# Performance work log

Hardware: AMD Instinct MI355X
Metric: run time of the kernel (lower is better)

Reference implementation:

```python
import jax, jax.numpy as jnp
import numpy as np

B, T, D = 2, 2048, 1024
NH, DH = 16, 64  # inner = NH*DH = D
SCALE_INIT = 0.02


def setup_inputs() -> dict:
    key = jax.random.key(0)
    kx, kq, kk, kv, ko = jax.random.split(key, 5)
    return {
        "x": jax.random.normal(kx, (B, T, D), dtype=jnp.float32),
        "Wq": jax.random.normal(kq, (D, NH * DH), dtype=jnp.float32) * SCALE_INIT,
        "Wk": jax.random.normal(kk, (D, NH * DH), dtype=jnp.float32) * SCALE_INIT,
        "Wv": jax.random.normal(kv, (D, NH * DH), dtype=jnp.float32) * SCALE_INIT,
        "Wo": jax.random.normal(ko, (NH * DH, D), dtype=jnp.float32) * SCALE_INIT,
    }


def reference(x, Wq, Wk, Wv, Wo):
    # x: (B, T, D)
    b, t, _ = x.shape

    def split_heads(h):
        # (B, T, NH*DH) -> (B, NH, T, DH)
        return h.reshape(b, t, NH, DH).transpose(0, 2, 1, 3)

    q = split_heads(x @ Wq)
    k = split_heads(x @ Wk)
    v = split_heads(x @ Wv)

    scale = jnp.asarray(1.0 / np.sqrt(DH), dtype=x.dtype)
    # The per-chunk loop in the original is mathematically equivalent to
    # full causal attention: each query row attends to keys with k_pos <= q_pos.
    scores = jnp.einsum("bhqd,bhkd->bhqk", q, k) * scale  # (B, NH, T, T)
    causal_mask = jnp.arange(t)[None, :] > jnp.arange(t)[:, None]  # k_pos > q_pos
    scores = jnp.where(causal_mask, -jnp.inf, scores)
    attn = jax.nn.softmax(scores, axis=-1)
    attn = jnp.nan_to_num(attn)  # matches torch.nan_to_num (no fully-masked rows in causal case)
    o = jnp.einsum("bhqk,bhkd->bhqd", attn, v)  # (B, NH, T, DH)
    o = o.transpose(0, 2, 1, 3).reshape(b, t, NH * DH)  # merge heads
    return o @ Wo  # (B, T, D)
```

## Files before the change

kernel.cpp:

```cpp
#include <hip/hip_runtime.h>
#include <hip/hip_bf16.h>
#include <string.h>

#define Bsz 2
#define Tsz 2048
#define Dsz 1024
#define NHsz 16
#define Msz (Bsz*Tsz)

typedef unsigned short bfu;
typedef __attribute__((ext_vector_type(8))) short short8;
typedef __attribute__((ext_vector_type(4))) short short4v;
typedef __attribute__((ext_vector_type(4))) float floatx4;

__device__ __forceinline__ bfu f2bf(float f) {
  unsigned int u = __builtin_bit_cast(unsigned int, f);
  u += 0x7fffu + ((u >> 16) & 1u);
  return (bfu)(u >> 16);
}

__device__ __forceinline__ short4v pack4bf(float a, float b, float c_, float d) {
  __hip_bfloat162 h01 = __float22bfloat162_rn(make_float2(a, b));
  __hip_bfloat162 h23 = __float22bfloat162_rn(make_float2(c_, d));
  uint2 uu;
  memcpy(&uu.x, &h01, 4);
  memcpy(&uu.y, &h23, 4);
  return __builtin_bit_cast(short4v, uu);
}

__device__ __forceinline__ short8 pack8bf(float4 a, float4 b) {
  __hip_bfloat162 h0 = __float22bfloat162_rn(make_float2(a.x, a.y));
  __hip_bfloat162 h1 = __float22bfloat162_rn(make_float2(a.z, a.w));
  __hip_bfloat162 h2 = __float22bfloat162_rn(make_float2(b.x, b.y));
  __hip_bfloat162 h3 = __float22bfloat162_rn(make_float2(b.z, b.w));
  uint4 u;
  memcpy(&u.x, &h0, 4); memcpy(&u.y, &h1, 4);
  memcpy(&u.z, &h2, 4); memcpy(&u.w, &h3, 4);
  return __builtin_bit_cast(short8, u);
}

__device__ __forceinline__ void async16(const void* g, void* l) {
  void* gnc = (void*)g;
  __builtin_amdgcn_global_load_lds((__attribute__((address_space(1))) void*)gnc,
                                   (__attribute__((address_space(3))) void*)l,
                                   16, 0, 0);
}

__global__ __launch_bounds__(256) void transpose_w(const float* __restrict__ W0, const float* __restrict__ W1,
                                                   const float* __restrict__ W2, const float* __restrict__ W3,
                                                   bfu* __restrict__ wt) {
  __shared__ float tile[32][33];
  const float* W = blockIdx.z == 0 ? W0 : blockIdx.z == 1 ? W1 : blockIdx.z == 2 ? W2 : W3;
  const float s = (blockIdx.z == 0) ? 0.18033688011112042f : 1.0f;
  bfu* WT = wt + (size_t)blockIdx.z * Dsz * Dsz;
  int tx = threadIdx.x, ty = threadIdx.y;
  int kb = blockIdx.y * 32, nb = blockIdx.x * 32;
#pragma unroll
  for (int i = 0; i < 4; ++i)
    tile[ty + i*8][tx] = W[(size_t)(kb + ty + i*8) * Dsz + nb + tx];
  __syncthreads();
#pragma unroll
  for (int i = 0; i < 4; ++i)
    WT[(size_t)(nb + ty + i*8) * Dsz + kb + tx] = f2bf(tile[tx][ty + i*8] * s);
}

template <bool F32OUT, bool AF32, int NT>
__global__ __launch_bounds__(256) void gemm128(const void* __restrict__ Ain, const bfu* __restrict__ Bt0,
                                               void* __restrict__ C0, int K, int N,
                                               size_t strideB, size_t strideC) {
  constexpr int NJ = NT / 32;
  const int tid = threadIdx.x, wave = tid >> 6, lane = tid & 63;
  const int g = lane >> 4, c = lane & 15;
  const int m0 = blockIdx.y * 128, n0 = blockIdx.x * NT;
  const bfu* Bt = Bt0 + strideB * blockIdx.z;
  __shared__ bfu smem[4096 + NT * 32];
  bfu* As = smem;
  bfu* Bs = smem + 4096;
  floatx4 acc[4][NJ] = {};
  const int srow = lane >> 2, scol = (lane & 3) * 8;
  const bfu* gB = Bt + (size_t)(n0 + srow) * K + scol;
  const int wm = (wave >> 1) * 64, wn = (wave & 1) * (NT / 2);

  short8 areg[2];
  if (AF32) {
#pragma unroll
    for (int cc = 0; cc < 2; ++cc) {
      const float* pa = (const float*)Ain +
          (size_t)(m0 + (wave*2 + cc)*16 + srow) * K + scol;
      areg[cc] = pack8bf(((const float4*)pa)[0], ((const float4*)pa)[1]);
    }
  }
  const bfu* gA = AF32 ? nullptr : (const bfu*)Ain + (size_t)(m0 + srow) * K + scol;

  for (int k0 = 0; k0 < K; k0 += 32) {
    __syncthreads();
#pragma unroll
    for (int cc = 0; cc < 2; ++cc) {
      const int chunk = wave * 2 + cc;
      if (AF32) *(short8*)&As[chunk * 512 + lane * 8] = areg[cc];
      else      async16(gA + (size_t)chunk * 16 * K + k0, &As[chunk * 512]);
    }
#pragma unroll
    for (int cc = 0; cc < NT/64; ++cc) {
      const int chunk = wave * (NT/64) + cc;
      async16(gB + (size_t)chunk * 16 * K + k0, &Bs[chunk * 512]);
    }
    __syncthreads();
    if (AF32 && k0 + 32 < K) {
#pragma unroll
      for (int cc = 0; cc < 2; ++cc) {
        const float* pa = (const float*)Ain +
            (size_t)(m0 + (wave*2 + cc)*16 + srow) * K + (k0 + 32) + scol;
        areg[cc] = pack8bf(((const float4*)pa)[0], ((const float4*)pa)[1]);
      }
    }
    short8 afr[4], bfr[NJ];
#pragma unroll
    for (int t = 0; t < 4; ++t) afr[t] = *(const short8*)&As[(wm + t*16 + c) * 32 + g * 8];
#pragma unroll
    for (int t = 0; t < NJ; ++t) bfr[t] = *(const short8*)&Bs[(wn + t*16 + c) * 32 + g * 8];
#pragma unroll
    for (int i = 0; i < 4; ++i)
#pragma unroll
      for (int j = 0; j < NJ; ++j)
        acc[i][j] = __builtin_amdgcn_mfma_f32_16x16x32_bf16(afr[i], bfr[j], acc[i][j], 0, 0, 0);
  }

  const bool vtrans = (!F32OUT) && (NT == 128) && (blockIdx.z == 2);
  if (vtrans) {
    bfu* vtp = (bfu*)C0 + (size_t)2 * strideC;
#pragma unroll
    for (int p = 0; p < 2; ++p) {
      __syncthreads();
      if ((wave & 1) == p) {
#pragma unroll
        for (int i = 0; i < 4; ++i)
#pragma unroll
          for (int j = 0; j < NJ; ++j) {
            const int nl = j*16 + c;
            const int mg = ((wm + i*16) >> 3) + (g >> 1);
            const int phys = nl * 128 + ((mg ^ (nl & 15)) << 3) + ((g & 1) << 2);
            *(short4v*)&smem[phys] = pack4bf(acc[i][j][0], acc[i][j][1],
                                             acc[i][j][2], acc[i][j][3]);
          }
      }
      __syncthreads();
      const int h_ = (n0 + p * 64) >> 6;
      bfu* dst = vtp + ((size_t)((m0 >> 11) * 16 + h_) * 64) * Tsz + (m0 & 2047);
#pragma unroll
      for (int s = 0; s < 4; ++s) {
        const int nl = s * 16 + (tid >> 4);
        const int me = (tid & 15) << 3;
        const int phys = nl * 128 + (((me >> 3) ^ (nl & 15)) << 3);
        *(short8*)&dst[(size_t)nl * Tsz + me] = *(const short8*)&smem[phys];
      }
    }
    return;
  }

#pragma unroll
  for (int i = 0; i < 4; ++i) {
#pragma unroll
    for (int j = 0; j < NJ; ++j) {
      const int m = m0 + wm + i*16 + g*4;
      const int n = n0 + wn + j*16 + c;
#pragma unroll
      for (int r = 0; r < 4; ++r) {
        float v = acc[i][j][r];
        if (F32OUT) ((float*)C0)[(size_t)(m + r) * N + n] = v;
        else        ((bfu*)C0)[strideC * blockIdx.z + (size_t)(m + r) * N + n] = f2bf(v);
      }
    }
  }
}

__global__ __launch_bounds__(256, 2) void attn_kernel(const bfu* __restrict__ qkv,
                                                      bfu* __restrict__ obuf) {
  const int tid = threadIdx.x, wave = tid >> 6, lane = tid & 63;
  const int g = (lane >> 4) & 3, c = lane & 15, c7 = c & 7;
  const int bh = blockIdx.y, b = bh >> 4, h = bh & 15;
  const size_t hb = (size_t)b * Tsz * Dsz + h * 64;
  const bfu* Qp = qkv + hb;
  const bfu* Kp = qkv + (size_t)Msz * Dsz + hb;
  const bfu* Vt = qkv + (size_t)2 * Msz * Dsz + (size_t)bh * 64 * Tsz;

  __shared__ bfu Ks[128 * 64];
  __shared__ bfu Vs[64 * 128];
  __shared__ bfu Ps[4][16 * 128];

  const int kst_row = lane >> 3;
  const int kst_off = ((lane & 7) ^ kst_row) << 3;
  const int vst_row = lane >> 4;

  for (int half = 0; half < 2; ++half) {
    const int j = half ? (31 - (int)blockIdx.x) : (int)blockIdx.x;
    const int qw = j * 64 + wave * 16;
    const int ktm = j >> 1;

    short8 bq[2];
#pragma unroll
    for (int kk = 0; kk < 2; ++kk)
      bq[kk] = *(const short8*)(Qp + (size_t)(qw + c) * Dsz + kk * 32 + g * 8);

    floatx4 acc[4] = {};
    float mi = -3.0e38f, li = 0.0f;

    for (int kt = 0; kt <= ktm; ++kt) {
      __syncthreads();
#pragma unroll
      for (int cc = 0; cc < 4; ++cc) {
        const int ch = wave * 4 + cc;
        async16(Kp + (size_t)(kt * 128 + ch * 8 + kst_row) * Dsz + kst_off, &Ks[ch * 512]);
        const int drow = ch * 4 + vst_row;
        async16(Vt + (size_t)drow * Tsz + kt * 128 + (((lane & 15) ^ (drow & 7)) << 3), &Vs[ch * 512]);
      }
      __syncthreads();

      floatx4 st[8] = {};
#pragma unroll
      for (int kk = 0; kk < 2; ++kk)
#pragma unroll
        for (int mk = 0; mk < 8; ++mk) {
          const short8 kf = *(const short8*)&Ks[(mk * 16 + c) * 64 + (((kk * 4 + g) ^ c7) << 3)];
          st[mk] = __builtin_amdgcn_mfma_f32_16x16x32_bf16(kf, bq[kk], st[mk], 0, 0, 0);
        }

      if (kt == ktm) {
#pragma unroll
        for (int mk = 0; mk < 8; ++mk) {
          const int keyb = kt * 128 + mk * 16 + g * 4;
#pragma unroll
          for (int r = 0; r < 4; ++r)
            if (keyb + r > qw + c) st[mk][r] = -1.0e38f;
        }
      }

      float mloc = -3.0e38f;
#pragma unroll
      for (int mk = 0; mk < 8; ++mk)
#pragma unroll
        for (int r = 0; r < 4; ++r) mloc = fmaxf(mloc, st[mk][r]);
      mloc = fmaxf(mloc, __shfl_xor(mloc, 16));
      mloc = fmaxf(mloc, __shfl_xor(mloc, 32));
      const float mnew = fmaxf(mi, mloc);
      const float alpha = exp2f(mi - mnew);
      mi = mnew;
      float sum = 0.0f;
#pragma unroll
      for (int mk = 0; mk < 8; ++mk) {
        short4v pk;
#pragma unroll
        for (int r = 0; r < 4; ++r) {
          const float p = exp2f(st[mk][r] - mnew);
          sum += p;
          pk[r] = (short)f2bf(p);
        }
        *(short4v*)&Ps[wave][c * 128 + (((mk * 2 + (g >> 1)) ^ c7) << 3) + ((g & 1) << 2)] = pk;
      }
      sum += __shfl_xor(sum, 16);
      sum += __shfl_xor(sum, 32);
      li = li * alpha + sum;

      float al[4];
#pragma unroll
      for (int r = 0; r < 4; ++r) al[r] = __shfl(alpha, (lane & 48) | (g * 4 + r));
#pragma unroll
      for (int nd = 0; nd < 4; ++nd)
#pragma unroll
        for (int r = 0; r < 4; ++r) acc[nd][r] *= al[r];

#pragma unroll
      for (int kc = 0; kc < 4; ++kc) {
        const int sl = ((kc * 4 + g) ^ c7) << 3;
        const short8 pf = *(const short8*)&Ps[wave][c * 128 + sl];
#pragma unroll
        for (int nd = 0; nd < 4; ++nd) {
          const short8 vf = *(const short8*)&Vs[(nd * 16 + c) * 128 + sl];
          acc[nd] = __builtin_amdgcn_mfma_f32_16x16x32_bf16(pf, vf, acc[nd], 0, 0, 0);
        }
      }
    }

    float inv[4];
#pragma unroll
    for (int r = 0; r < 4; ++r) inv[r] = 1.0f / __shfl(li, (lane & 48) | (g * 4 + r));
#pragma unroll
    for (int nd = 0; nd < 4; ++nd)
#pragma unroll
      for (int r = 0; r < 4; ++r)
        obuf[(size_t)(b * Tsz + qw + g * 4 + r) * Dsz + h * 64 + nd * 16 + c] =
            f2bf(acc[nd][r] * inv[r]);
  }
}

extern "C" void kernel_launch(void* const* d_in, const int* in_sizes, int n_in,
                              void* d_out, int out_size, void* d_ws, size_t ws_size,
                              hipStream_t stream) {
  const float* x  = (const float*)d_in[0];
  const float* Wq = (const float*)d_in[1];
  const float* Wk = (const float*)d_in[2];
  const float* Wv = (const float*)d_in[3];
  const float* Wo = (const float*)d_in[4];
  float* out = (float*)d_out;

  bfu* wt   = (bfu*)d_ws;
  bfu* qkv  = wt  + (size_t)4 * Dsz * Dsz;
  bfu* obuf = qkv + (size_t)3 * Msz * Dsz;

  transpose_w<<<dim3(32, 32, 4), dim3(32, 8), 0, stream>>>(Wq, Wk, Wv, Wo, wt);
  gemm128<false, true, 128><<<dim3(Dsz / 128, Msz / 128, 3), dim3(256), 0, stream>>>(
      (const void*)x, wt, (void*)qkv, Dsz, Dsz, (size_t)Dsz * Dsz, (size_t)Msz * Dsz);
  attn_kernel<<<dim3(16, Bsz * NHsz), dim3(256), 0, stream>>>(qkv, obuf);
  gemm128<true, false, 64><<<dim3(Dsz / 64, Msz / 128, 1), dim3(256), 0, stream>>>(
      (const void*)obuf, wt + (size_t)3 * Dsz * Dsz, (void*)out, Dsz, Dsz,
      (size_t)0, (size_t)0);
}
```

Baseline: 198.9 us.

## Widen attention key tiles to 256 with causal block skipping; deepen QKV GEMM k-step

The attention kernel now stages 256 keys and values per iteration instead of 128. Within a tile it computes scores and P·V only for 16-key sub-blocks that are not fully masked, and applies the causal mask only to blocks on the diagonal. The QKV projection GEMM is split into its own kernel with a 64-wide k step and swizzled shared memory, which halves the number of barrier iterations. The output GEMM becomes a separate specialised kernel. The larger attention tiles double LDS use, which may lower occupancy, and the dynamic per-block bounds add branching.

Measured after the change: 231.9 us. +16.6%, slower.

```diff
diff --git a/kernel.cpp b/kernel.cpp
--- a/kernel.cpp
+++ b/kernel.cpp
@@ -64,71 +64,63 @@
     WT[(size_t)(nb + ty + i*8) * Dsz + kb + tx] = f2bf(tile[tx][ty + i*8] * s);
 }
 
-template <bool F32OUT, bool AF32, int NT>
-__global__ __launch_bounds__(256) void gemm128(const void* __restrict__ Ain, const bfu* __restrict__ Bt0,
-                                               void* __restrict__ C0, int K, int N,
-                                               size_t strideB, size_t strideC) {
-  constexpr int NJ = NT / 32;
+__global__ __launch_bounds__(256) void gemm_qkv(const float* __restrict__ x,
+                                                const bfu* __restrict__ Bt0,
+                                                bfu* __restrict__ C0,
+                                                size_t strideB, size_t strideC) {
   const int tid = threadIdx.x, wave = tid >> 6, lane = tid & 63;
-  const int g = lane >> 4, c = lane & 15;
-  const int m0 = blockIdx.y * 128, n0 = blockIdx.x * NT;
+  const int g = lane >> 4, c = lane & 15, c7 = c & 7;
+  const int m0 = blockIdx.y * 128, n0 = blockIdx.x * 128;
   const bfu* Bt = Bt0 + strideB * blockIdx.z;
-  __shared__ bfu smem[4096 + NT * 32];
-  bfu* As = smem;
-  bfu* Bs = smem + 4096;
-  floatx4 acc[4][NJ] = {};
-  const int srow = lane >> 2, scol = (lane & 3) * 8;
-  const bfu* gB = Bt + (size_t)(n0 + srow) * K + scol;
-  const int wm = (wave >> 1) * 64, wn = (wave & 1) * (NT / 2);
-
-  short8 areg[2];
-  if (AF32) {
-#pragma unroll
-    for (int cc = 0; cc < 2; ++cc) {
-      const float* pa = (const float*)Ain +
-          (size_t)(m0 + (wave*2 + cc)*16 + srow) * K + scol;
-      areg[cc] = pack8bf(((const float4*)pa)[0], ((const float4*)pa)[1]);
-    }
-  }
-  const bfu* gA = AF32 ? nullptr : (const bfu*)Ain + (size_t)(m0 + srow) * K + scol;
-
-  for (int k0 = 0; k0 < K; k0 += 32) {
+  __shared__ bfu As[128 * 64];
+  __shared__ bfu Bs[128 * 64];
+  floatx4 acc[4][4] = {};
+  const int srow = lane >> 3;
+  const int sgr  = lane & 7;
+  const int sw_off = ((sgr ^ srow) << 3);
+  const int wm = (wave >> 1) * 64, wn = (wave & 1) * 64;
+
+  short8 areg[4];
+#pragma unroll
+  for (int cc = 0; cc < 4; ++cc) {
+    const float* pa = x + (size_t)(m0 + (wave*4 + cc)*8 + srow) * Dsz + sgr*8;
+    areg[cc] = pack8bf(((const float4*)pa)[0], ((const float4*)pa)[1]);
+  }
+
+  for (int k0 = 0; k0 < Dsz; k0 += 64) {
     __syncthreads();
 #pragma unroll
-    for (int cc = 0; cc < 2; ++cc) {
-      const int chunk = wave * 2 + cc;
-      if (AF32) *(short8*)&As[chunk * 512 + lane * 8] = areg[cc];
-      else      async16(gA + (size_t)chunk * 16 * K + k0, &As[chunk * 512]);
-    }
-#pragma unroll
-    for (int cc = 0; cc < NT/64; ++cc) {
-      const int chunk = wave * (NT/64) + cc;
-      async16(gB + (size_t)chunk * 16 * K + k0, &Bs[chunk * 512]);
+    for (int cc = 0; cc < 4; ++cc) {
+      const int ch = wave * 4 + cc;
+      *(short8*)&As[ch * 512 + srow * 64 + sw_off] = areg[cc];
+      async16(Bt + (size_t)(n0 + ch*8 + srow) * Dsz + k0 + sw_off, &Bs[ch * 512]);
     }
     __syncthreads();
-    if (AF32 && k0 + 32 < K) {
-#pragma unroll
-      for (int cc = 0; cc < 2; ++cc) {
-        const float* pa = (const float*)Ain +
-            (size_t)(m0 + (wave*2 + cc)*16 + srow) * K + (k0 + 32) + scol;
+    if (k0 + 64 < Dsz) {
+#pragma unroll
+      for (int cc = 0; cc < 4; ++cc) {
+        const float* pa = x + (size_t)(m0 + (wave*4 + cc)*8 + srow) * Dsz + (k0 + 64) + sgr*8;
         areg[cc] = pack8bf(((const float4*)pa)[0], ((const float4*)pa)[1]);
       }
     }
-    short8 afr[4], bfr[NJ];
-#pragma unroll
-    for (int t = 0; t < 4; ++t) afr[t] = *(const short8*)&As[(wm + t*16 + c) * 32 + g * 8];
-#pragma unroll
-    for (int t = 0; t < NJ; ++t) bfr[t] = *(const short8*)&Bs[(wn + t*16 + c) * 32 + g * 8];
-#pragma unroll
-    for (int i = 0; i < 4; ++i)
-#pragma unroll
-      for (int j = 0; j < NJ; ++j)
-        acc[i][j] = __builtin_amdgcn_mfma_f32_16x16x32_bf16(afr[i], bfr[j], acc[i][j], 0, 0, 0);
-  }
-
-  const bool vtrans = (!F32OUT) && (NT == 128) && (blockIdx.z == 2);
-  if (vtrans) {
-    bfu* vtp = (bfu*)C0 + (size_t)2 * strideC;
+#pragma unroll
+    for (int kk = 0; kk < 2; ++kk) {
+      short8 afr[4], bfr[4];
+#pragma unroll
+      for (int t = 0; t < 4; ++t) {
+        afr[t] = *(const short8*)&As[(wm + t*16 + c) * 64 + (((kk*4 + g) ^ c7) << 3)];
+        bfr[t] = *(const short8*)&Bs[(wn + t*16 + c) * 64 + (((kk*4 + g) ^ c7) << 3)];
+      }
+#pragma unroll
+      for (int i = 0; i < 4; ++i)
+#pragma unroll
+        for (int j = 0; j < 4; ++j)
+          acc[i][j] = __builtin_amdgcn_mfma_f32_16x16x32_bf16(afr[i], bfr[j], acc[i][j], 0, 0, 0);
+    }
+  }
+
+  if (blockIdx.z == 2) {
+    bfu* vtp = C0 + (size_t)2 * strideC;
 #pragma unroll
     for (int p = 0; p < 2; ++p) {
       __syncthreads();
@@ -136,12 +128,12 @@
 #pragma unroll
         for (int i = 0; i < 4; ++i)
 #pragma unroll
-          for (int j = 0; j < NJ; ++j) {
+          for (int j = 0; j < 4; ++j) {
             const int nl = j*16 + c;
             const int mg = ((wm + i*16) >> 3) + (g >> 1);
             const int phys = nl * 128 + ((mg ^ (nl & 15)) << 3) + ((g & 1) << 2);
-            *(short4v*)&smem[phys] = pack4bf(acc[i][j][0], acc[i][j][1],
-                                             acc[i][j][2], acc[i][j][3]);
+            *(short4v*)&As[phys] = pack4bf(acc[i][j][0], acc[i][j][1],
+                                           acc[i][j][2], acc[i][j][3]);
           }
       }
       __syncthreads();
@@ -152,26 +144,65 @@
         const int nl = s * 16 + (tid >> 4);
         const int me = (tid & 15) << 3;
         const int phys = nl * 128 + (((me >> 3) ^ (nl & 15)) << 3);
-        *(short8*)&dst[(size_t)nl * Tsz + me] = *(const short8*)&smem[phys];
+        *(short8*)&dst[(size_t)nl * Tsz + me] = *(const short8*)&As[phys];
       }
     }
     return;
   }
-
-#pragma unroll
-  for (int i = 0; i < 4; ++i) {
-#pragma unroll
-    for (int j = 0; j < NJ; ++j) {
+#pragma unroll
+  for (int i = 0; i < 4; ++i)
+#pragma unroll
+    for (int j = 0; j < 4; ++j) {
       const int m = m0 + wm + i*16 + g*4;
       const int n = n0 + wn + j*16 + c;
 #pragma unroll
-      for (int r = 0; r < 4; ++r) {
-        float v = acc[i][j][r];
-        if (F32OUT) ((float*)C0)[(size_t)(m + r) * N + n] = v;
-        else        ((bfu*)C0)[strideC * blockIdx.z + (size_t)(m + r) * N + n] = f2bf(v);
-      }
-    }
-  }
+      for (int r = 0; r < 4; ++r)
+        C0[strideC * blockIdx.z + (size_t)(m + r) * Dsz + n] = f2bf(acc[i][j][r]);
+    }
+}
+
+__global__ __launch_bounds__(256) void gemm_out(const bfu* __restrict__ A, const bfu* __restrict__ Bt,
+                                                float* __restrict__ C0) {
+  const int tid = threadIdx.x, wave = tid >> 6, lane = tid & 63;
+  const int g = lane >> 4, c = lane & 15;
+  const int m0 = blockIdx.y * 128, n0 = blockIdx.x * 64;
+  __shared__ bfu As[128 * 32];
+  __shared__ bfu Bs[64 * 32];
+  floatx4 acc[4][2] = {};
+  const int srow = lane >> 2, scol = (lane & 3) * 8;
+  const bfu* gA = A  + (size_t)(m0 + srow) * Dsz + scol;
+  const bfu* gB = Bt + (size_t)(n0 + srow) * Dsz + scol;
+  const int wm = (wave >> 1) * 64, wn = (wave & 1) * 32;
+  for (int k0 = 0; k0 < Dsz; k0 += 32) {
+    __syncthreads();
+#pragma unroll
+    for (int cc = 0; cc < 2; ++cc) {
+      const int chunk = wave * 2 + cc;
+      async16(gA + (size_t)chunk * 16 * Dsz + k0, &As[chunk * 512]);
+    }
+    async16(gB + (size_t)wave * 16 * Dsz + k0, &Bs[wave * 512]);
+    __syncthreads();
+    short8 afr[4], bfr[2];
+#pragma unroll
+    for (int t = 0; t < 4; ++t) afr[t] = *(const short8*)&As[(wm + t*16 + c) * 32 + g * 8];
+#pragma unroll
+    for (int t = 0; t < 2; ++t) bfr[t] = *(const short8*)&Bs[(wn + t*16 + c) * 32 + g * 8];
+#pragma unroll
+    for (int i = 0; i < 4; ++i)
+#pragma unroll
+      for (int j = 0; j < 2; ++j)
+        acc[i][j] = __builtin_amdgcn_mfma_f32_16x16x32_bf16(afr[i], bfr[j], acc[i][j], 0, 0, 0);
+  }
+#pragma unroll
+  for (int i = 0; i < 4; ++i)
+#pragma unroll
+    for (int j = 0; j < 2; ++j) {
+      const int m = m0 + wm + i*16 + g*4;
+      const int n = n0 + wn + j*16 + c;
+#pragma unroll
+      for (int r = 0; r < 4; ++r)
+        C0[(size_t)(m + r) * Dsz + n] = acc[i][j][r];
+    }
 }
 
 __global__ __launch_bounds__(256, 2) void attn_kernel(const bfu* __restrict__ qkv,
@@ -184,18 +215,19 @@
   const bfu* Kp = qkv + (size_t)Msz * Dsz + hb;
   const bfu* Vt = qkv + (size_t)2 * Msz * Dsz + (size_t)bh * 64 * Tsz;
 
-  __shared__ bfu Ks[128 * 64];
-  __shared__ bfu Vs[64 * 128];
+  __shared__ bfu Ks[256 * 64];
+  __shared__ bfu Vs[64 * 256];
   __shared__ bfu Ps[4][16 * 128];
 
   const int kst_row = lane >> 3;
   const int kst_off = ((lane & 7) ^ kst_row) << 3;
-  const int vst_row = lane >> 4;
+  const int vrow_in = lane >> 5;
+  const int vgr     = lane & 31;
 
   for (int half = 0; half < 2; ++half) {
     const int j = half ? (31 - (int)blockIdx.x) : (int)blockIdx.x;
     const int qw = j * 64 + wave * 16;
-    const int ktm = j >> 1;
+    const int ktm = (j * 64 + 63) >> 8;
 
     short8 bq[2];
 #pragma unroll
@@ -208,87 +240,110 @@
     for (int kt = 0; kt <= ktm; ++kt) {
       __syncthreads();
 #pragma unroll
-      for (int cc = 0; cc < 4; ++cc) {
-        const int ch = wave * 4 + cc;
-        async16(Kp + (size_t)(kt * 128 + ch * 8 + kst_row) * Dsz + kst_off, &Ks[ch * 512]);
-        const int drow = ch * 4 + vst_row;
-        async16(Vt + (size_t)drow * Tsz + kt * 128 + (((lane & 15) ^ (drow & 7)) << 3), &Vs[ch * 512]);
+      for (int cc = 0; cc < 8; ++cc) {
+        const int ch = wave * 8 + cc;
+        async16(Kp + (size_t)(kt*256 + ch*8 + kst_row) * Dsz + kst_off, &Ks[ch * 512]);
+        const int drow = ch * 2 + vrow_in;
+        async16(Vt + (size_t)drow * Tsz + kt*256 + ((vgr ^ (drow & 7)) << 3), &Vs[ch * 512]);
       }
       __syncthreads();
 
-      floatx4 st[8] = {};
-#pragma unroll
-      for (int kk = 0; kk < 2; ++kk)
-#pragma unroll
-        for (int mk = 0; mk < 8; ++mk) {
-          const short8 kf = *(const short8*)&Ks[(mk * 16 + c) * 64 + (((kk * 4 + g) ^ c7) << 3)];
-          st[mk] = __builtin_amdgcn_mfma_f32_16x16x32_bf16(kf, bq[kk], st[mk], 0, 0, 0);
+      const int kbase = kt * 256;
+      const int rem = qw + 16 - kbase;
+      const int mk_hi = rem >= 256 ? 16 : ((rem + 15) >> 4);
+      const int mask_lo = max(0, (qw + 1 - kbase) >> 4);
+
+      floatx4 st[16];
+#pragma unroll
+      for (int mk = 0; mk < 16; ++mk) {
+        if (mk < mk_hi) {
+          const short8 kf0 = *(const short8*)&Ks[(mk*16 + c) * 64 + ((g ^ c7) << 3)];
+          const short8 kf1 = *(const short8*)&Ks[(mk*16 + c) * 64 + (((4 + g) ^ c7) << 3)];
+          floatx4 z = {};
+          z = __builtin_amdgcn_mfma_f32_16x16x32_bf16(kf0, bq[0], z, 0, 0, 0);
+          st[mk] = __builtin_amdgcn_mfma_f32_16x16x32_bf16(kf1, bq[1], st[mk] = z, 0, 0, 0);
+          if (mk >= mask_lo) {
+            const int keyb = kbase + mk*16 + g*4;
+#pragma unroll
+            for (int r = 0; r < 4; ++r)
+              if (keyb + r > qw + c) st[mk][r] = -1.0e38f;
+          }
         }
-
-      if (kt == ktm) {
-#pragma unroll
-        for (int mk = 0; mk < 8; ++mk) {
-          const int keyb = kt * 128 + mk * 16 + g * 4;
-#pragma unroll
-          for (int r = 0; r < 4; ++r)
-            if (keyb + r > qw + c) st[mk][r] = -1.0e38f;
+      }
+
+      float mloc = -3.0e38f;
+#pragma unroll
+      for (int mk = 0; mk < 16; ++mk)
+        if (mk < mk_hi) {
+#pragma unroll
+          for (int r = 0; r < 4; ++r) mloc = fmaxf(mloc, st[mk][r]);
         }
-      }
-
-      float mloc = -3.0e38f;
-#pragma unroll
-      for (int mk = 0; mk < 8; ++mk)
-#pragma unroll
-        for (int r = 0; r < 4; ++r) mloc = fmaxf(mloc, st[mk][r]);
       mloc = fmaxf(mloc, __shfl_xor(mloc, 16));
       mloc = fmaxf(mloc, __shfl_xor(mloc, 32));
       const float mnew = fmaxf(mi, mloc);
       const float alpha = exp2f(mi - mnew);
       mi = mnew;
+      float al[4];
+#pragma unroll
+      for (int r = 0; r < 4; ++r) al[r] = __shfl(alpha, (lane & 48) | (g*4 + r));
+#pragma unroll
+      for (int nd = 0; nd < 4; ++nd)
+#pragma unroll
+        for (int r = 0; r < 4; ++r) acc[nd][r] *= al[r];
+
       float sum = 0.0f;
 #pragma unroll
-      for (int mk = 0; mk < 8; ++mk) {
-        short4v pk;
-#pragma unroll
-        for (int r = 0; r < 4; ++r) {
-          const float p = exp2f(st[mk][r] - mnew);
-          sum += p;
-          pk[r] = (short)f2bf(p);
+      for (int h2 = 0; h2 < 2; ++h2) {
+        const int rem2 = rem - h2 * 128;
+        const int lmk_hi = rem2 >= 128 ? 8 : (rem2 <= 0 ? 0 : ((rem2 + 15) >> 4));
+        const int kc_hi  = rem2 >= 128 ? 4 : (rem2 <= 0 ? 0 : ((rem2 + 31) >> 5));
+        if (kc_hi > 0) {
+#pragma unroll
+          for (int lm = 0; lm < 8; ++lm) {
+            const int pofs = c * 128 + (((lm*2 + (g >> 1)) ^ c7) << 3) + ((g & 1) << 2);
+            if (lm < lmk_hi) {
+              const int mk = h2*8 + lm;
+              short4v pk;
+#pragma unroll
+              for (int r = 0; r < 4; ++r) {
+                const float p = exp2f(st[mk][r] - mnew);
+                sum += p;
+                pk[r] = (short)f2bf(p);
+              }
+              *(short4v*)&Ps[wave][pofs] = pk;
+            } else if (lm < kc_hi * 2) {
+              short4v z4 = {};
+              *(short4v*)&Ps[wave][pofs] = z4;
+            }
+          }
+#pragma unroll
+          for (int kc = 0; kc < 4; ++kc) {
+            if (kc < kc_hi) {
+              const int sl = ((kc*4 + g) ^ c7) << 3;
+              const short8 pf = *(const short8*)&Ps[wave][c * 128 + sl];
+#pragma unroll
+              for (int nd = 0; nd < 4; ++nd) {
+                const short8 vf =
+                    *(const short8*)&Vs[(nd*16 + c) * 256 + (((h2*16 + kc*4 + g) ^ c7) << 3)];
+                acc[nd] = __builtin_amdgcn_mfma_f32_16x16x32_bf16(pf, vf, acc[nd], 0, 0, 0);
+              }
+            }
+          }
         }
-        *(short4v*)&Ps[wave][c * 128 + (((mk * 2 + (g >> 1)) ^ c7) << 3) + ((g & 1) << 2)] = pk;
       }
       sum += __shfl_xor(sum, 16);
       sum += __shfl_xor(sum, 32);
       li = li * alpha + sum;
-
-      float al[4];
-#pragma unroll
-      for (int r = 0; r < 4; ++r) al[r] = __shfl(alpha, (lane & 48) | (g * 4 + r));
-#pragma unroll
-      for (int nd = 0; nd < 4; ++nd)
-#pragma unroll
-        for (int r = 0; r < 4; ++r) acc[nd][r] *= al[r];
-
-#pragma unroll
-      for (int kc = 0; kc < 4; ++kc) {
-        const int sl = ((kc * 4 + g) ^ c7) << 3;
-        const short8 pf = *(const short8*)&Ps[wave][c * 128 + sl];
-#pragma unroll
-        for (int nd = 0; nd < 4; ++nd) {
-          const short8 vf = *(const short8*)&Vs[(nd * 16 + c) * 128 + sl];
-          acc[nd] = __builtin_amdgcn_mfma_f32_16x16x32_bf16(pf, vf, acc[nd], 0, 0, 0);
-        }
-      }
     }
 
     float inv[4];
 #pragma unroll
-    for (int r = 0; r < 4; ++r) inv[r] = 1.0f / __shfl(li, (lane & 48) | (g * 4 + r));
+    for (int r = 0; r < 4; ++r) inv[r] = 1.0f / __shfl(li, (lane & 48) | (g*4 + r));
 #pragma unroll
     for (int nd = 0; nd < 4; ++nd)
 #pragma unroll
       for (int r = 0; r < 4; ++r)
-        obuf[(size_t)(b * Tsz + qw + g * 4 + r) * Dsz + h * 64 + nd * 16 + c] =
+        obuf[(size_t)(b * Tsz + qw + g*4 + r) * Dsz + h * 64 + nd*16 + c] =
             f2bf(acc[nd][r] * inv[r]);
   }
 }
@@ -308,10 +363,9 @@
   bfu* obuf = qkv + (size_t)3 * Msz * Dsz;
 
   transpose_w<<<dim3(32, 32, 4), dim3(32, 8), 0, stream>>>(Wq, Wk, Wv, Wo, wt);
-  gemm128<false, true, 128><<<dim3(Dsz / 128, Msz / 128, 3), dim3(256), 0, stream>>>(
-      (const void*)x, wt, (void*)qkv, Dsz, Dsz, (size_t)Dsz * Dsz, (size_t)Msz * Dsz);
+  gemm_qkv<<<dim3(Dsz / 128, Msz / 128, 3), dim3(256), 0, stream>>>(
+      x, wt, qkv, (size_t)Dsz * Dsz, (size_t)Msz * Dsz);
   attn_kernel<<<dim3(16, Bsz * NHsz), dim3(256), 0, stream>>>(qkv, obuf);
-  gemm128<true, false, 64><<<dim3(Dsz / 64, Msz / 128, 1), dim3(256), 0, stream>>>(
-      (const void*)obuf, wt + (size_t)3 * Dsz * Dsz, (void*)out, Dsz, Dsz,
-      (size_t)0, (size_t)0);
-}
+  gemm_out<<<dim3(Dsz / 64, Msz / 128, 1), dim3(256), 0, stream>>>(
+      obuf, wt + (size_t)3 * Dsz * Dsz, out);
+}
```

## Split attention into one q-tile per block with 1D grid and smaller P buffer

Applied to the files above, without the earlier changes.

The attention kernel no longer processes two paired query tiles per block. It launches 1024 blocks, each handling a single 64-row query tile, and orders them in quads so that long and short causal tiles interleave across the grid. The per-wave P staging buffer is halved by writing and consuming probabilities in two 64-key halves, and launch bounds are raised to allow 4 blocks per CU, aiming at higher occupancy and better load spread. In exchange, Q loads and block setup are repeated more often, and the balance now depends on how the hardware schedules blocks rather than on the fixed pairing.

New measurement: 199.9 us. No clear change (+0.5%).

```diff
diff --git a/kernel.cpp b/kernel.cpp
--- a/kernel.cpp
+++ b/kernel.cpp
@@ -174,11 +174,14 @@
   }
 }
 
-__global__ __launch_bounds__(256, 2) void attn_kernel(const bfu* __restrict__ qkv,
+__global__ __launch_bounds__(256, 4) void attn_kernel(const bfu* __restrict__ qkv,
                                                       bfu* __restrict__ obuf) {
   const int tid = threadIdx.x, wave = tid >> 6, lane = tid & 63;
   const int g = (lane >> 4) & 3, c = lane & 15, c7 = c & 7;
-  const int bh = blockIdx.y, b = bh >> 4, h = bh & 15;
+  const int quad = blockIdx.x >> 8, p = blockIdx.x & 255;
+  const int bh = p & 31, jj = p >> 5;
+  const int j = (quad == 0) ? jj : (quad == 1) ? (15 - jj) : (quad == 2) ? (16 + jj) : (31 - jj);
+  const int b = bh >> 4, h = bh & 15;
   const size_t hb = (size_t)b * Tsz * Dsz + h * 64;
   const bfu* Qp = qkv + hb;
   const bfu* Kp = qkv + (size_t)Msz * Dsz + hb;
@@ -186,111 +189,112 @@
 
   __shared__ bfu Ks[128 * 64];
   __shared__ bfu Vs[64 * 128];
-  __shared__ bfu Ps[4][16 * 128];
+  __shared__ bfu Ps[4][16 * 64];
 
   const int kst_row = lane >> 3;
   const int kst_off = ((lane & 7) ^ kst_row) << 3;
   const int vst_row = lane >> 4;
 
-  for (int half = 0; half < 2; ++half) {
-    const int j = half ? (31 - (int)blockIdx.x) : (int)blockIdx.x;
-    const int qw = j * 64 + wave * 16;
-    const int ktm = j >> 1;
-
-    short8 bq[2];
+  const int qw = j * 64 + wave * 16;
+  const int ktm = j >> 1;
+
+  short8 bq[2];
+#pragma unroll
+  for (int kk = 0; kk < 2; ++kk)
+    bq[kk] = *(const short8*)(Qp + (size_t)(qw + c) * Dsz + kk * 32 + g * 8);
+
+  floatx4 acc[4] = {};
+  float mi = -3.0e38f, li = 0.0f;
+
+  for (int kt = 0; kt <= ktm; ++kt) {
+    __syncthreads();
+#pragma unroll
+    for (int cc = 0; cc < 4; ++cc) {
+      const int ch = wave * 4 + cc;
+      async16(Kp + (size_t)(kt * 128 + ch * 8 + kst_row) * Dsz + kst_off, &Ks[ch * 512]);
+      const int drow = ch * 4 + vst_row;
+      async16(Vt + (size_t)drow * Tsz + kt * 128 + (((lane & 15) ^ (drow & 7)) << 3), &Vs[ch * 512]);
+    }
+    __syncthreads();
+
+    floatx4 st[8] = {};
 #pragma unroll
     for (int kk = 0; kk < 2; ++kk)
-      bq[kk] = *(const short8*)(Qp + (size_t)(qw + c) * Dsz + kk * 32 + g * 8);
-
-    floatx4 acc[4] = {};
-    float mi = -3.0e38f, li = 0.0f;
-
-    for (int kt = 0; kt <= ktm; ++kt) {
-      __syncthreads();
-#pragma unroll
-      for (int cc = 0; cc < 4; ++cc) {
-        const int ch = wave * 4 + cc;
-        async16(Kp + (size_t)(kt * 128 + ch * 8 + kst_row) * Dsz + kst_off, &Ks[ch * 512]);
-        const int drow = ch * 4 + vst_row;
-        async16(Vt + (size_t)drow * Tsz + kt * 128 + (((lane & 15) ^ (drow & 7)) << 3), &Vs[ch * 512]);
-      }
-      __syncthreads();
-
-      floatx4 st[8] = {};
-#pragma unroll
-      for (int kk = 0; kk < 2; ++kk)
-#pragma unroll
-        for (int mk = 0; mk < 8; ++mk) {
-          const short8 kf = *(const short8*)&Ks[(mk * 16 + c) * 64 + (((kk * 4 + g) ^ c7) << 3)];
-          st[mk] = __builtin_amdgcn_mfma_f32_16x16x32_bf16(kf, bq[kk], st[mk], 0, 0, 0);
+#pragma unroll
+      for (int mk = 0; mk < 8; ++mk) {
+        const short8 kf = *(const short8*)&Ks[(mk * 16 + c) * 64 + (((kk * 4 + g) ^ c7) << 3)];
+        st[mk] = __builtin_amdgcn_mfma_f32_16x16x32_bf16(kf, bq[kk], st[mk], 0, 0, 0);
+      }
+
+    if (kt == ktm) {
+#pragma unroll
+      for (int mk = 0; mk < 8; ++mk) {
+        const int keyb = kt * 128 + mk * 16 + g * 4;
+#pragma unroll
+        for (int r = 0; r < 4; ++r)
+          if (keyb + r > qw + c) st[mk][r] = -1.0e38f;
+      }
+    }
+
+    float mloc = -3.0e38f;
+#pragma unroll
+    for (int mk = 0; mk < 8; ++mk)
+#pragma unroll
+      for (int r = 0; r < 4; ++r) mloc = fmaxf(mloc, st[mk][r]);
+    mloc = fmaxf(mloc, __shfl_xor(mloc, 16));
+    mloc = fmaxf(mloc, __shfl_xor(mloc, 32));
+    const float mnew = fmaxf(mi, mloc);
+    const float alpha = exp2f(mi - mnew);
+    mi = mnew;
+
+    float al[4];
+#pragma unroll
+    for (int r = 0; r < 4; ++r) al[r] = __shfl(alpha, (lane & 48) | (g * 4 + r));
+#pragma unroll
+    for (int nd = 0; nd < 4; ++nd)
+#pragma unroll
+      for (int r = 0; r < 4; ++r) acc[nd][r] *= al[r];
+
+    float sum = 0.0f;
+#pragma unroll
+    for (int hh = 0; hh < 2; ++hh) {
+#pragma unroll
+      for (int lm = 0; lm < 4; ++lm) {
+        const int mk = hh * 4 + lm;
+        short4v pk;
+#pragma unroll
+        for (int r = 0; r < 4; ++r) {
+          const float pv = exp2f(st[mk][r] - mnew);
+          sum += pv;
+          pk[r] = (short)f2bf(pv);
         }
-
-      if (kt == ktm) {
-#pragma unroll
-        for (int mk = 0; mk < 8; ++mk) {
-          const int keyb = kt * 128 + mk * 16 + g * 4;
-#pragma unroll
-          for (int r = 0; r < 4; ++r)
-            if (keyb + r > qw + c) st[mk][r] = -1.0e38f;
-        }
-      }
-
-      float mloc = -3.0e38f;
-#pragma unroll
-      for (int mk = 0; mk < 8; ++mk)
-#pragma unroll
-        for (int r = 0; r < 4; ++r) mloc = fmaxf(mloc, st[mk][r]);
-      mloc = fmaxf(mloc, __shfl_xor(mloc, 16));
-      mloc = fmaxf(mloc, __shfl_xor(mloc, 32));
-      const float mnew = fmaxf(mi, mloc);
-      const float alpha = exp2f(mi - mnew);
-      mi = mnew;
-      float sum = 0.0f;
-#pragma unroll
-      for (int mk = 0; mk < 8; ++mk) {
-        short4v pk;
-#pragma unroll
-        for (int r = 0; r < 4; ++r) {
-          const float p = exp2f(st[mk][r] - mnew);
-          sum += p;
-          pk[r] = (short)f2bf(p);
-        }
-        *(short4v*)&Ps[wave][c * 128 + (((mk * 2 + (g >> 1)) ^ c7) << 3) + ((g & 1) << 2)] = pk;
-      }
-      sum += __shfl_xor(sum, 16);
-      sum += __shfl_xor(sum, 32);
-      li = li * alpha + sum;
-
-      float al[4];
-#pragma unroll
-      for (int r = 0; r < 4; ++r) al[r] = __shfl(alpha, (lane & 48) | (g * 4 + r));
-#pragma unroll
-      for (int nd = 0; nd < 4; ++nd)
-#pragma unroll
-        for (int r = 0; r < 4; ++r) acc[nd][r] *= al[r];
-
-#pragma unroll
-      for (int kc = 0; kc < 4; ++kc) {
-        const int sl = ((kc * 4 + g) ^ c7) << 3;
-        const short8 pf = *(const short8*)&Ps[wave][c * 128 + sl];
+        *(short4v*)&Ps[wave][c * 64 + (((lm * 2 + (g >> 1)) ^ c7) << 3) + ((g & 1) << 2)] = pk;
+      }
+#pragma unroll
+      for (int kcl = 0; kcl < 2; ++kcl) {
+        const int kc = hh * 2 + kcl;
+        const short8 pf = *(const short8*)&Ps[wave][c * 64 + (((kcl * 4 + g) ^ c7) << 3)];
 #pragma unroll
         for (int nd = 0; nd < 4; ++nd) {
-          const short8 vf = *(const short8*)&Vs[(nd * 16 + c) * 128 + sl];
+          const short8 vf = *(const short8*)&Vs[(nd * 16 + c) * 128 + (((kc * 4 + g) ^ c7) << 3)];
           acc[nd] = __builtin_amdgcn_mfma_f32_16x16x32_bf16(pf, vf, acc[nd], 0, 0, 0);
         }
       }
     }
-
-    float inv[4];
-#pragma unroll
-    for (int r = 0; r < 4; ++r) inv[r] = 1.0f / __shfl(li, (lane & 48) | (g * 4 + r));
-#pragma unroll
-    for (int nd = 0; nd < 4; ++nd)
-#pragma unroll
-      for (int r = 0; r < 4; ++r)
-        obuf[(size_t)(b * Tsz + qw + g * 4 + r) * Dsz + h * 64 + nd * 16 + c] =
-            f2bf(acc[nd][r] * inv[r]);
-  }
+    sum += __shfl_xor(sum, 16);
+    sum += __shfl_xor(sum, 32);
+    li = li * alpha + sum;
+  }
+
+  float inv[4];
+#pragma unroll
+  for (int r = 0; r < 4; ++r) inv[r] = 1.0f / __shfl(li, (lane & 48) | (g * 4 + r));
+#pragma unroll
+  for (int nd = 0; nd < 4; ++nd)
+#pragma unroll
+    for (int r = 0; r < 4; ++r)
+      obuf[(size_t)(b * Tsz + qw + g * 4 + r) * Dsz + h * 64 + nd * 16 + c] =
+          f2bf(acc[nd][r] * inv[r]);
 }
 
 extern "C" void kernel_launch(void* const* d_in, const int* in_sizes, int n_in,
@@ -310,7 +314,7 @@
   transpose_w<<<dim3(32, 32, 4), dim3(32, 8), 0, stream>>>(Wq, Wk, Wv, Wo, wt);
   gemm128<false, true, 128><<<dim3(Dsz / 128, Msz / 128, 3), dim3(256), 0, stream>>>(
       (const void*)x, wt, (void*)qkv, Dsz, Dsz, (size_t)Dsz * Dsz, (size_t)Msz * Dsz);
-  attn_kernel<<<dim3(16, Bsz * NHsz), dim3(256), 0, stream>>>(qkv, obuf);
+  attn_kernel<<<dim3(1024), dim3(256), 0, stream>>>(qkv, obuf);
   gemm128<true, false, 64><<<dim3(Dsz / 64, Msz / 128, 1), dim3(256), 0, stream>>>(
       (const void*)obuf, wt + (size_t)3 * Dsz * Dsz, (void*)out, Dsz, Dsz,
       (size_t)0, (size_t)0);
```
